# Kernel optimization log

Hardware: AMD Instinct MI355X
Metric: run time of the kernel (lower is better)

The kernel has to match this reference:

```python
import jax, jax.numpy as jnp
import numpy as np
from jax import lax

B, C, H, W = 32, 3, 32, 32
F = 160      # nr_filters
NBLK = 5     # nr_resnet
NMIX = 10    # mixture components
P = 100      # nr_params for 3-channel input


def concat_elu(x):
    return jax.nn.elu(jnp.concatenate([x, -x], axis=1))


def _conv(x, w, b, pad):
    y = lax.conv_general_dilated(x, w, (1, 1), pad, dimension_numbers=('NCHW', 'OIHW', 'NCHW'))
    return y + b[None, :, None, None]


def ds_conv(x, w, b):
    # down-shifted conv: causal in vertical direction
    kh, kw = w.shape[2], w.shape[3]
    return _conv(x, w, b, ((kh - 1, 0), ((kw - 1) // 2, (kw - 1) // 2)))


def dr_conv(x, w, b):
    # down-right-shifted conv: causal in vertical and horizontal direction
    kh, kw = w.shape[2], w.shape[3]
    return _conv(x, w, b, ((kh - 1, 0), (kw - 1, 0)))


def down_shift(x):
    return jnp.pad(x, ((0, 0), (0, 0), (1, 0), (0, 0)))[:, :, :-1, :]


def right_shift(x):
    return jnp.pad(x, ((0, 0), (0, 0), (0, 0), (1, 0)))[:, :, :, :-1]


def nin(x, w, b):
    return jnp.einsum('bchw,oc->bohw', x, w) + b[None, :, None, None]


def gated_resnet(x, a, c1w, c1b, ninw, ninb, c2w, c2b, conv_fn):
    c1 = conv_fn(concat_elu(x), c1w, c1b)
    if a is not None:
        c1 = c1 + nin(concat_elu(a), ninw, ninb)
    c2 = conv_fn(concat_elu(c1), c2w, c2b)  # 2F channels
    g1, g2 = jnp.split(c2, 2, axis=1)
    return x + g1 * jax.nn.sigmoid(g2)


def dmll(x, l):
    # discretized mixture logistic loss; x: [B,C,H,W] in [-1,1], l: [B,P,H,W]
    x = jnp.transpose(x, (0, 2, 3, 1))   # BHWC
    l = jnp.transpose(l, (0, 2, 3, 1))   # BHWP
    logit_probs = l[..., :NMIX]
    rest = l[..., NMIX:].reshape(l.shape[:3] + (C, 3 * NMIX))
    means = rest[..., :NMIX]
    log_scales = jnp.maximum(rest[..., NMIX:2 * NMIX], -7.0)
    coeffs = jnp.tanh(rest[..., 2 * NMIX:])
    xe = x[..., None]                    # BHWC1
    m1 = means[..., 0, :]
    m2 = means[..., 1, :] + coeffs[..., 0, :] * xe[..., 0, :]
    m3 = means[..., 2, :] + coeffs[..., 1, :] * xe[..., 0, :] + coeffs[..., 2, :] * xe[..., 1, :]
    means = jnp.stack([m1, m2, m3], axis=3)  # BHWCM
    centered = xe - means
    inv_stdv = jnp.exp(-log_scales)
    plus_in = inv_stdv * (centered + 1.0 / 255.0)
    min_in = inv_stdv * (centered - 1.0 / 255.0)
    cdf_delta = jax.nn.sigmoid(plus_in) - jax.nn.sigmoid(min_in)
    log_cdf_plus = plus_in - jax.nn.softplus(plus_in)
    log_one_minus_cdf_min = -jax.nn.softplus(min_in)
    mid_in = inv_stdv * centered
    log_pdf_mid = mid_in - log_scales - 2.0 * jax.nn.softplus(mid_in)
    log_probs = jnp.where(xe < -0.999, log_cdf_plus,
                jnp.where(xe > 0.999, log_one_minus_cdf_min,
                jnp.where(cdf_delta > 1e-5, jnp.log(jnp.maximum(cdf_delta, 1e-12)),
                          log_pdf_mid - np.float32(np.log(127.5)))))
    log_probs = log_probs.sum(axis=3) + jax.nn.log_softmax(logit_probs, axis=-1)
    return -jnp.sum(jax.nn.logsumexp(log_probs, axis=-1))


def _forward(samples, w_u_init, b_u_init, w_ul_d, b_ul_d, w_ul_dr, b_ul_dr,
             u_c1_w, u_c1_b, u_c2_w, u_c2_b,
             ul_c1_w, ul_c1_b, ul_nin_w, ul_nin_b, ul_c2_w, ul_c2_b,
             nin_out_w, nin_out_b):
    x = samples * 2.0 - 1.0
    # PixelCNN++ pads a constant ones channel onto the input
    xp = jnp.concatenate([x, jnp.ones_like(x[:, :1])], axis=1)
    u = down_shift(ds_conv(xp, w_u_init, b_u_init))
    ul = down_shift(ds_conv(xp, w_ul_d, b_ul_d)) + right_shift(dr_conv(xp, w_ul_dr, b_ul_dr))
    for i in range(NBLK):
        u = gated_resnet(u, None, u_c1_w[i], u_c1_b[i], None, None, u_c2_w[i], u_c2_b[i], ds_conv)
        ul = gated_resnet(ul, u, ul_c1_w[i], ul_c1_b[i], ul_nin_w[i], ul_nin_b[i], ul_c2_w[i], ul_c2_b[i], dr_conv)
    params = nin(jax.nn.elu(ul), nin_out_w, nin_out_b)  # [B,P,H,W]
    return -dmll(x, params)  # log_prob (scalar, summed over batch/pixels)


def setup_inputs() -> dict:
    key = jax.random.key(0)
    ks = jax.random.split(key, 12)
    s = 0.05
    return {
        'samples': jax.random.uniform(ks[0], (B, C, H, W), jnp.float32),
        'w_u_init': jax.random.normal(ks[1], (F, C + 1, 2, 3), jnp.float32) * s,
        'b_u_init': jnp.zeros((F,), jnp.float32),
        'w_ul_d': jax.random.normal(ks[2], (F, C + 1, 1, 3), jnp.float32) * s,
        'b_ul_d': jnp.zeros((F,), jnp.float32),
        'w_ul_dr': jax.random.normal(ks[3], (F, C + 1, 2, 1), jnp.float32) * s,
        'b_ul_dr': jnp.zeros((F,), jnp.float32),
        'u_c1_w': jax.random.normal(ks[4], (NBLK, F, 2 * F, 2, 3), jnp.float32) * s,
        'u_c1_b': jnp.zeros((NBLK, F), jnp.float32),
        'u_c2_w': jax.random.normal(ks[5], (NBLK, 2 * F, 2 * F, 2, 3), jnp.float32) * s,
        'u_c2_b': jnp.zeros((NBLK, 2 * F), jnp.float32),
        'ul_c1_w': jax.random.normal(ks[6], (NBLK, F, 2 * F, 2, 2), jnp.float32) * s,
        'ul_c1_b': jnp.zeros((NBLK, F), jnp.float32),
        'ul_nin_w': jax.random.normal(ks[7], (NBLK, F, 2 * F), jnp.float32) * s,
        'ul_nin_b': jnp.zeros((NBLK, F), jnp.float32),
        'ul_c2_w': jax.random.normal(ks[8], (NBLK, 2 * F, 2 * F, 2, 2), jnp.float32) * s,
        'ul_c2_b': jnp.zeros((NBLK, 2 * F), jnp.float32),
        'nin_out_w': jax.random.normal(ks[9], (P, F), jnp.float32) * s,
        'nin_out_b': jnp.zeros((P,), jnp.float32),
    }


def reference(samples, w_u_init, b_u_init, w_ul_d, b_ul_d, w_ul_dr, b_ul_dr,
              u_c1_w, u_c1_b, u_c2_w, u_c2_b,
              ul_c1_w, ul_c1_b, ul_nin_w, ul_nin_b, ul_c2_w, ul_c2_b,
              nin_out_w, nin_out_b):
    return _forward(samples, w_u_init, b_u_init, w_ul_d, b_ul_d, w_ul_dr, b_ul_dr,
                    u_c1_w, u_c1_b, u_c2_w, u_c2_b,
                    ul_c1_w, ul_c1_b, ul_nin_w, ul_nin_b, ul_c2_w, ul_c2_b,
                    nin_out_w, nin_out_b)
```

## Files before the change

kernel.cpp:

```cpp
#include <hip/hip_runtime.h>
#include <math.h>

#define BZ 32
#define FCH 160
#define NMIX 10
#define PCH 100

typedef __attribute__((ext_vector_type(8))) short bf16x8;
typedef __attribute__((ext_vector_type(8))) unsigned short u16x8;
typedef __attribute__((ext_vector_type(4))) unsigned short u16x4;
typedef __attribute__((ext_vector_type(4))) float f32x4;

__device__ __forceinline__ unsigned short f2bf(float f) {
    union { float f; unsigned u; } x; x.f = f;
    return (unsigned short)((x.u + 0x7FFFu + ((x.u >> 16) & 1u)) >> 16);
}
__device__ __forceinline__ void elupair(float v, float& e0, float& e1) {
    if (v > 0.f) { e0 = v; e1 = expm1f(-v); }
    else         { e0 = expm1f(v); e1 = -v; }
}
__device__ __forceinline__ int fsw(int p) { return (p + (p >> 2)) & 3; }
__device__ __forceinline__ int swz(int p, int seg) {
    return p * 32 + ((seg ^ fsw(p)) << 3);
}
__device__ __forceinline__ void load_lds16(const unsigned short* g, unsigned short* l) {
    __builtin_amdgcn_global_load_lds(
        (const __attribute__((address_space(1))) unsigned int*)g,
        (__attribute__((address_space(3))) unsigned int*)l, 16, 0, 0);
}

__global__ __launch_bounds__(256) void repack_k(
    const float* __restrict__ w, unsigned short* __restrict__ wb,
    int Cout, int Cin, int NT, int ILV)
{
    __shared__ float ws[1920];
    const int o = blockIdx.x;
    const int nb = blockIdx.y;
    const int CoutPad = gridDim.x;
    const int n = Cin * NT;
    unsigned short* dst = wb + (size_t)(nb * CoutPad + o) * n;
    if (o >= Cout) {
        for (int e = threadIdx.x; e < n; e += 256) dst[e] = 0;
        return;
    }
    const float* src = w + (size_t)(nb * Cout + o) * n;
    for (int e = threadIdx.x; e < n; e += 256) ws[e] = src[e];
    __syncthreads();
    const int half = Cin >> 1;
    for (int e = threadIdx.x; e < n; e += 256) {
        int tap = e / Cin;
        int k = e - tap * Cin;
        int csrc = ILV ? ((k & 1) ? (half + (k >> 1)) : (k >> 1)) : k;
        dst[e] = f2bf(ws[csrc * NT + tap]);
    }
}

__global__ __launch_bounds__(256) void init_both_k(
    const float* __restrict__ smp,
    const float* __restrict__ wu_g, const float* __restrict__ bu_g,
    const float* __restrict__ wd_g, const float* __restrict__ bd_g,
    const float* __restrict__ wr_g, const float* __restrict__ br_g,
    float* __restrict__ u, float* __restrict__ ul,
    unsigned short* __restrict__ ceu, unsigned short* __restrict__ ceul,
    float* __restrict__ zg)
{
    __shared__ float wU[160 * 24];
    __shared__ float wD[160 * 12];
    __shared__ float wR[160 * 8];
    __shared__ float bU[160], bD[160], bR[160];
    __shared__ float X[3][4][34];

    const int tid = threadIdx.x;
    const int i = blockIdx.x;
    const int b = blockIdx.y;

    if (i == 0 && b == 0 && tid < 128) {
        f32x4 z = {0.f, 0.f, 0.f, 0.f};
        ((f32x4*)zg)[tid] = z;
    }

    for (int e = tid; e < 160 * 24; e += 256) wU[e] = wu_g[e];
    for (int e = tid; e < 160 * 12; e += 256) wD[e] = wd_g[e];
    for (int e = tid; e < 160 * 8;  e += 256) wR[e] = wr_g[e];
    if (tid < 160) { bU[tid] = bu_g[tid]; bD[tid] = bd_g[tid]; bR[tid] = br_g[tid]; }
    for (int e = tid; e < 3 * 4 * 34; e += 256) {
        int col = e % 34;
        int c = (e / 34) & 3;
        int rs = e / (34 * 4);
        int r = i - 2 + rs;
        int jj = col - 1;
        float v = 0.f;
        if ((unsigned)r < 32u && (unsigned)jj < 32u)
            v = (c < 3) ? (smp[(((size_t)b * 3 + c) << 10) + (r << 5) + jj] * 2.f - 1.f)
                        : 1.f;
        X[rs][c][col] = v;
    }
    __syncthreads();
    if (tid >= 160) return;
    const int o = tid;

    float wu_r[24], wd_r[12], wr_r[8];
#pragma unroll
    for (int q = 0; q < 24; ++q) wu_r[q] = wU[o * 24 + q];
#pragma unroll
    for (int q = 0; q < 12; ++q) wd_r[q] = wD[o * 12 + q];
#pragma unroll
    for (int q = 0; q < 8; ++q)  wr_r[q] = wR[o * 8 + q];
    const float bu_v = (i > 0) ? bU[o] : 0.f;
    const float bd_v = (i >= 1) ? bD[o] : 0.f;
    const float br_v = bR[o];

    for (int j = 0; j < 32; ++j) {
        float su = 0.f, sd = 0.f, sr = 0.f;
#pragma unroll
        for (int c = 0; c < 4; ++c) {
            float x00 = X[0][c][j], x01 = X[0][c][j + 1], x02 = X[0][c][j + 2];
            float x10 = X[1][c][j], x11 = X[1][c][j + 1], x12 = X[1][c][j + 2];
            float x20 = X[2][c][j];
            su += wu_r[c * 6 + 0] * x00 + wu_r[c * 6 + 1] * x01 + wu_r[c * 6 + 2] * x02
                + wu_r[c * 6 + 3] * x10 + wu_r[c * 6 + 4] * x11 + wu_r[c * 6 + 5] * x12;
            sd += wd_r[c * 3 + 0] * x10 + wd_r[c * 3 + 1] * x11 + wd_r[c * 3 + 2] * x12;
            sr += wr_r[c * 2 + 0] * x10 + wr_r[c * 2 + 1] * x20;
        }
        float uv = (i > 0) ? (su + bu_v) : 0.f;
        float ulv = sd + bd_v + sr + ((j >= 1) ? br_v : 0.f);

        size_t base = (size_t)((b << 10) | (i << 5) | j);
        u[base * 160 + o] = uv;
        ul[base * 160 + o] = ulv;
        float e0, e1;
        elupair(uv, e0, e1);
        unsigned pu = (unsigned)f2bf(e0) | ((unsigned)f2bf(e1) << 16);
        *(unsigned*)(ceu + base * 320 + 2 * o) = pu;
        elupair(ulv, e0, e1);
        unsigned pl = (unsigned)f2bf(e0) | ((unsigned)f2bf(e1) << 16);
        *(unsigned*)(ceul + base * 320 + 2 * o) = pl;
    }
}

template<int KH, int KW, int PT, int PL, bool DUAL, bool GATE, int MBLK>
__device__ __forceinline__ void conv_body(
    int bid, unsigned short* smem,
    const unsigned short* __restrict__ cein,
    const unsigned short* __restrict__ wb,
    const unsigned short* __restrict__ cein2,
    const unsigned short* __restrict__ wb2,
    const float* __restrict__ bias, const float* __restrict__ bias2,
    float* __restrict__ resid,
    unsigned short* __restrict__ ceout,
    const unsigned short* __restrict__ zguard)
{
    constexpr int NT = KH * KW;
    constexpr int RW = 8 + KH - 1;
    constexpr int CW = 32 + KW - 1;
    constexpr int MTILES = MBLK / 16;
    constexpr int MSH = (MBLK == 32) ? 5 : 6;
    constexpr int NSA = NT * MBLK / 64;
    constexpr int NSB = (RW * CW * 4 + 255) / 256;
    constexpr int BSZ = NSB * 64 * 32;

    unsigned short* bs = smem;
    unsigned short* wsm = smem + BSZ;

    const int tid = threadIdx.x;
    const int wv = tid >> 6;
    const int lane = tid & 63;
    const int l16 = lane & 15;
    const int quad = lane >> 4;

    const int q8 = bid >> 3;
    const int yt = (bid & 7) * 16 + q8 / 5;
    const int m0 = (q8 % 5) * 32;
    const int bimg = yt >> 2;
    const int rowbase = (yt & 3) * 8;

    const int sd = lane & 3;
    const int lr = lane >> 2;

    const unsigned short* srcA[NSA];
#pragma unroll
    for (int it = 0; it < NSA; ++it) {
        int row = it * 64 + wv * 16 + lr;
        int tap = row >> MSH;
        int mm = row & (MBLK - 1);
        int o = GATE ? (mm < 32 ? m0 + mm : 128 + m0 + mm) : (m0 + mm);
        int ss = sd ^ fsw(row);
        srcA[it] = wb + ((size_t)o * NT + tap) * 320 + ss * 8;
    }
    const unsigned short* srcB[NSB];
#pragma unroll
    for (int it = 0; it < NSB; ++it) {
        int p = it * 64 + wv * 16 + lr;
        int r = p / CW;
        int c = p - r * CW;
        int grow = rowbase + r - PT;
        int gcol = c - PL;
        int ss = sd ^ fsw(p);
        bool ok = (p < RW * CW) && ((unsigned)grow < 32u) && ((unsigned)gcol < 32u);
        srcB[it] = ok ? cein + (size_t)(((bimg << 10) | (grow << 5) | gcol)) * 320 + ss * 8
                      : zguard;
    }

    f32x4 acc[MTILES][4];
#pragma unroll
    for (int mt = 0; mt < MTILES; ++mt)
#pragma unroll
        for (int ng = 0; ng < 4; ++ng)
#pragma unroll
            for (int r = 0; r < 4; ++r) acc[mt][ng][r] = 0.f;

    for (int k0 = 0; k0 < 320; k0 += 32) {
        __syncthreads();
#pragma unroll
        for (int it = 0; it < NSB; ++it)
            load_lds16(srcB[it] + k0, &bs[(it * 64 + wv * 16) * 32]);
#pragma unroll
        for (int it = 0; it < NSA; ++it)
            load_lds16(srcA[it] + k0, &wsm[(it * 64 + wv * 16) * 32]);
        __syncthreads();
#pragma unroll
        for (int tap = 0; tap < NT; ++tap) {
            const int kh = tap / KW, kw = tap % KW;
            bf16x8 af[MTILES];
#pragma unroll
            for (int mt = 0; mt < MTILES; ++mt)
                af[mt] = *(const bf16x8*)&wsm[swz(tap * MBLK + mt * 16 + l16, quad)];
#pragma unroll
            for (int ng = 0; ng < 4; ++ng) {
                int rl = 2 * wv + (ng >> 1) + kh;
                int cc = (ng & 1) * 16 + l16 + kw;
                bf16x8 bfr = *(const bf16x8*)&bs[swz(rl * CW + cc, quad)];
#pragma unroll
                for (int mt = 0; mt < MTILES; ++mt)
                    acc[mt][ng] = __builtin_amdgcn_mfma_f32_16x16x32_bf16(af[mt], bfr, acc[mt][ng], 0, 0, 0);
            }
        }
    }

    if (DUAL) {
        const unsigned short* srcB2[4];
#pragma unroll
        for (int it = 0; it < 4; ++it) {
            int p2 = it * 64 + wv * 16 + lr;
            int r = p2 >> 5, c = p2 & 31;
            int ss = sd ^ fsw(p2);
            srcB2[it] = cein2 + (size_t)(((bimg << 10) | ((rowbase + r) << 5) | c)) * 320 + ss * 8;
        }
        int row2 = wv * 16 + lr;
        int mm2 = row2 & 31;
        const unsigned short* srcA2 =
            wb2 + (size_t)(m0 + mm2) * 320 + (sd ^ fsw(row2)) * 8;

        for (int k0 = 0; k0 < 320; k0 += 32) {
            __syncthreads();
#pragma unroll
            for (int it = 0; it < 4; ++it)
                load_lds16(srcB2[it] + k0, &bs[(it * 64 + wv * 16) * 32]);
            if (wv < 2)
                load_lds16(srcA2 + k0, &wsm[(wv * 16) * 32]);
            __syncthreads();
            bf16x8 af[MTILES];
#pragma unroll
            for (int mt = 0; mt < MTILES; ++mt)
                af[mt] = *(const bf16x8*)&wsm[swz(mt * 16 + l16, quad)];
#pragma unroll
            for (int ng = 0; ng < 4; ++ng) {
                int rl = 2 * wv + (ng >> 1);
                int cc = (ng & 1) * 16 + l16;
                bf16x8 bfr = *(const bf16x8*)&bs[swz(rl * 32 + cc, quad)];
#pragma unroll
                for (int mt = 0; mt < MTILES; ++mt)
                    acc[mt][ng] = __builtin_amdgcn_mfma_f32_16x16x32_bf16(af[mt], bfr, acc[mt][ng], 0, 0, 0);
            }
        }
    }

    constexpr int MOUT = GATE ? MTILES / 2 : MTILES;
#pragma unroll
    for (int mt = 0; mt < MOUT; ++mt) {
        int ob = m0 + mt * 16 + quad * 4;
        f32x4 bv = *(const f32x4*)(bias + ob);
        f32x4 bv2;
        if (DUAL) bv2 = *(const f32x4*)(bias2 + ob);
        f32x4 bg;
        if (GATE) bg = *(const f32x4*)(bias + ob + 160);
#pragma unroll
        for (int ng = 0; ng < 4; ++ng) {
            int i = rowbase + 2 * wv + (ng >> 1);
            int j = (ng & 1) * 16 + l16;
            size_t pb = (size_t)((bimg << 10) | (i << 5) | j);
            if (!GATE) {
                u16x8 st;
#pragma unroll
                for (int r = 0; r < 4; ++r) {
                    float v = acc[mt][ng][r] + bv[r] + (DUAL ? bv2[r] : 0.f);
                    float e0, e1; elupair(v, e0, e1);
                    st[2 * r] = f2bf(e0); st[2 * r + 1] = f2bf(e1);
                }
                *(u16x8*)(ceout + pb * 320 + 2 * ob) = st;
            } else {
                f32x4 rv = *(const f32x4*)(resid + pb * 160 + ob);
                u16x8 st;
#pragma unroll
                for (int r = 0; r < 4; ++r) {
                    float g1 = acc[mt][ng][r] + bv[r];
                    float g2 = acc[mt + MTILES / 2][ng][r] + bg[r];
                    float v = rv[r] + g1 / (1.f + expf(-g2));
                    rv[r] = v;
                    float e0, e1; elupair(v, e0, e1);
                    st[2 * r] = f2bf(e0); st[2 * r + 1] = f2bf(e1);
                }
                *(f32x4*)(resid + pb * 160 + ob) = rv;
                *(u16x8*)(ceout + pb * 320 + 2 * ob) = st;
            }
        }
    }
}

template<int KH, int KW, int PT, int PL, bool DUAL, bool GATE, int MBLK>
__global__ __launch_bounds__(256) void conv_single_k(
    const unsigned short* __restrict__ cein, const unsigned short* __restrict__ wb,
    const unsigned short* __restrict__ cein2, const unsigned short* __restrict__ wb2,
    const float* __restrict__ bias, const float* __restrict__ bias2,
    float* __restrict__ resid, unsigned short* __restrict__ ceout,
    const unsigned short* __restrict__ zguard)
{
    extern __shared__ __align__(16) unsigned short dsm[];
    conv_body<KH, KW, PT, PL, DUAL, GATE, MBLK>(
        blockIdx.x, dsm, cein, wb, cein2, wb2, bias, bias2, resid, ceout, zguard);
}

__global__ __launch_bounds__(256) void conv_fused_c1_k(
    const unsigned short* __restrict__ ceul, const unsigned short* __restrict__ wul1,
    const unsigned short* __restrict__ ceu_nin, const unsigned short* __restrict__ wnin,
    const float* __restrict__ bul1, const float* __restrict__ bnin,
    unsigned short* __restrict__ cec1ul,
    const unsigned short* __restrict__ ceu, const unsigned short* __restrict__ wu1,
    const float* __restrict__ bu1, unsigned short* __restrict__ cec1u,
    const unsigned short* __restrict__ zguard)
{
    extern __shared__ __align__(16) unsigned short dsm[];
    if (blockIdx.x < 640)
        conv_body<2, 2, 1, 1, true, false, 32>(
            blockIdx.x, dsm, ceul, wul1, ceu_nin, wnin, bul1, bnin, nullptr, cec1ul, zguard);
    else
        conv_body<2, 3, 1, 1, false, false, 32>(
            blockIdx.x - 640, dsm, ceu, wu1, nullptr, nullptr, bu1, nullptr, nullptr, cec1u, zguard);
}

__global__ __launch_bounds__(256) void conv_fused_c2_k(
    const unsigned short* __restrict__ cec1ul, const unsigned short* __restrict__ wul2,
    const float* __restrict__ bul2, float* __restrict__ ul_r,
    unsigned short* __restrict__ ceul,
    const unsigned short* __restrict__ cec1u, const unsigned short* __restrict__ wu2,
    const float* __restrict__ bu2, float* __restrict__ u_r,
    unsigned short* __restrict__ ceu,
    const unsigned short* __restrict__ zguard)
{
    extern __shared__ __align__(16) unsigned short dsm[];
    if (blockIdx.x < 640)
        conv_body<2, 2, 1, 1, false, true, 64>(
            blockIdx.x, dsm, cec1ul, wul2, nullptr, nullptr, bul2, nullptr, ul_r, ceul, zguard);
    else
        conv_body<2, 3, 1, 1, false, true, 64>(
            blockIdx.x - 640, dsm, cec1u, wu2, nullptr, nullptr, bu2, nullptr, u_r, ceu, zguard);
}

__global__ __launch_bounds__(256) void ninout_k(
    const float* __restrict__ ul, const unsigned short* __restrict__ wbn,
    const float* __restrict__ bias, float* __restrict__ params)
{
    constexpr int KCP = 40;
    __shared__ __align__(16) unsigned short bs[256 * KCP];
    __shared__ __align__(16) unsigned short wsm[32 * KCP];

    const int tid = threadIdx.x;
    const int wv = tid >> 6;
    const int lane = tid & 63;
    const int l16 = lane & 15;
    const int quad = lane >> 4;
    const int m0 = blockIdx.x * 32;
    const int bimg = blockIdx.y >> 2;
    const int rowbase = (blockIdx.y & 3) * 8;

    f32x4 acc[2][4];
#pragma unroll
    for (int mt = 0; mt < 2; ++mt)
#pragma unroll
        for (int ng = 0; ng < 4; ++ng)
#pragma unroll
            for (int r = 0; r < 4; ++r) acc[mt][ng][r] = 0.f;

    for (int k0 = 0; k0 < 160; k0 += 32) {
        __syncthreads();
        for (int e = tid; e < 256 * 8; e += 256) {
            int s = e & 7;
            int p = e >> 3;
            int pix = ((rowbase + (p >> 5)) << 5) | (p & 31);
            f32x4 xv = *(const f32x4*)(ul + (size_t)(((bimg << 10) | pix)) * 160 + k0 + s * 4);
            u16x4 st;
#pragma unroll
            for (int t = 0; t < 4; ++t) {
                float v = xv[t];
                st[t] = f2bf(v > 0.f ? v : expm1f(v));
            }
            *(u16x4*)(bs + p * KCP + s * 4) = st;
        }
        for (int e = tid; e < 32 * 4; e += 256) {
            int seg = e & 3;
            int mm = e >> 2;
            bf16x8 v = *(const bf16x8*)(wbn + (size_t)(m0 + mm) * 160 + k0 + seg * 8);
            *(bf16x8*)(wsm + mm * KCP + seg * 8) = v;
        }
        __syncthreads();
        bf16x8 af[2];
#pragma unroll
        for (int mt = 0; mt < 2; ++mt)
            af[mt] = *(const bf16x8*)&wsm[(mt * 16 + l16) * KCP + quad * 8];
#pragma unroll
        for (int ng = 0; ng < 4; ++ng) {
            int rl = 2 * wv + (ng >> 1);
            int cc = (ng & 1) * 16 + l16;
            bf16x8 bfr = *(const bf16x8*)&bs[(rl * 32 + cc) * KCP + quad * 8];
#pragma unroll
            for (int mt = 0; mt < 2; ++mt)
                acc[mt][ng] = __builtin_amdgcn_mfma_f32_16x16x32_bf16(af[mt], bfr, acc[mt][ng], 0, 0, 0);
        }
    }
#pragma unroll
    for (int mt = 0; mt < 2; ++mt)
#pragma unroll
        for (int ng = 0; ng < 4; ++ng) {
            int i = rowbase + 2 * wv + (ng >> 1);
            int j = (ng & 1) * 16 + l16;
            int pix = (i << 5) + j;
#pragma unroll
            for (int r = 0; r < 4; ++r) {
                int o = m0 + mt * 16 + quad * 4 + r;
                if (o < PCH)
                    params[(((size_t)bimg * PCH + o) << 10) + pix] = acc[mt][ng][r] + bias[o];
            }
        }
}

__device__ __forceinline__ float softplus_f(float v) {
    return fmaxf(v, 0.f) + log1pf(expf(-fabsf(v)));
}
__device__ __forceinline__ float sigmoid_f(float v) { return 1.f / (1.f + expf(-v)); }
__device__ __forceinline__ float lpterm(float x, float m, float ls) {
    float inv = expf(-ls);
    float cen = x - m;
    float plus = inv * (cen + 0.00392156862745098f);
    float minv = inv * (cen - 0.00392156862745098f);
    float cdf_delta = sigmoid_f(plus) - sigmoid_f(minv);
    float log_cdf_plus = plus - softplus_f(plus);
    float log_om = -softplus_f(minv);
    float mid = inv * cen;
    float log_pdf_mid = mid - ls - 2.f * softplus_f(mid);
    float inner = (cdf_delta > 1e-5f) ? logf(fmaxf(cdf_delta, 1e-12f))
                                      : (log_pdf_mid - 4.848116389675623f);
    return (x < -0.999f) ? log_cdf_plus : ((x > 0.999f) ? log_om : inner);
}

__global__ __launch_bounds__(256) void dmll_k(
    const float* __restrict__ smp, const float* __restrict__ params,
    float* __restrict__ partials)
{
    const int tid = threadIdx.x;
    const int n = tid & 15;
    const int ploc = tid >> 4;
    const int pix_g = blockIdx.x * 16 + ploc;
    const int b = pix_g >> 10;
    const int ij = pix_g & 1023;
    const float* P = params + ((size_t)b * PCH << 10) + ij;

    float x0 = smp[(((size_t)b * 3 + 0) << 10) + ij] * 2.f - 1.f;
    float x1 = smp[(((size_t)b * 3 + 1) << 10) + ij] * 2.f - 1.f;
    float x2 = smp[(((size_t)b * 3 + 2) << 10) + ij] * 2.f - 1.f;

    float logit = -1e30f;
    if (n < NMIX) logit = P[(size_t)n << 10];
    float mx = logit;
#pragma unroll
    for (int m = 1; m < 16; m <<= 1) mx = fmaxf(mx, __shfl_xor(mx, m, 16));
    float ex = (n < NMIX) ? expf(logit - mx) : 0.f;
    float se = ex;
#pragma unroll
    for (int m = 1; m < 16; m <<= 1) se += __shfl_xor(se, m, 16);
    float lse_logit = mx + logf(se);

    float lp = -1e30f;
    if (n < NMIX) {
        float mean0 = P[(size_t)(10 + n) << 10];
        float mean1 = P[(size_t)(40 + n) << 10];
        float mean2 = P[(size_t)(70 + n) << 10];
        float ls0 = fmaxf(P[(size_t)(20 + n) << 10], -7.f);
        float ls1 = fmaxf(P[(size_t)(50 + n) << 10], -7.f);
        float ls2 = fmaxf(P[(size_t)(80 + n) << 10], -7.f);
        float c0 = tanhf(P[(size_t)(30 + n) << 10]);
        float c1 = tanhf(P[(size_t)(60 + n) << 10]);
        float c2 = tanhf(P[(size_t)(90 + n) << 10]);
        float m0 = mean0;
        float m1 = mean1 + c0 * x0;
        float m2 = mean2 + c1 * x0 + c2 * x1;
        float s3 = lpterm(x0, m0, ls0) + lpterm(x1, m1, ls1) + lpterm(x2, m2, ls2);
        lp = s3 + logit - lse_logit;
    }
    float mx2 = lp;
#pragma unroll
    for (int m = 1; m < 16; m <<= 1) mx2 = fmaxf(mx2, __shfl_xor(mx2, m, 16));
    float e2 = (n < NMIX) ? expf(lp - mx2) : 0.f;
    float se2 = e2;
#pragma unroll
    for (int m = 1; m < 16; m <<= 1) se2 += __shfl_xor(se2, m, 16);
    float v = (n == 0) ? (mx2 + logf(se2)) : 0.f;

#pragma unroll
    for (int off = 32; off > 0; off >>= 1) v += __shfl_down(v, off);
    __shared__ float red[4];
    if ((tid & 63) == 0) red[tid >> 6] = v;
    __syncthreads();
    if (tid == 0) partials[blockIdx.x] = red[0] + red[1] + red[2] + red[3];
}

__global__ __launch_bounds__(256) void dmll_final_k(
    const float* __restrict__ partials, float* __restrict__ out)
{
    float v = 0.f;
    for (int k = threadIdx.x; k < 2048; k += 256) v += partials[k];
#pragma unroll
    for (int off = 32; off > 0; off >>= 1) v += __shfl_down(v, off);
    __shared__ float red[4];
    if ((threadIdx.x & 63) == 0) red[threadIdx.x >> 6] = v;
    __syncthreads();
    if (threadIdx.x == 0) out[0] = red[0] + red[1] + red[2] + red[3];
}

extern "C" void kernel_launch(void* const* d_in, const int* in_sizes, int n_in,
                              void* d_out, int out_size, void* d_ws, size_t ws_size,
                              hipStream_t stream)
{
    const float* samples   = (const float*)d_in[0];
    const float* w_u_init  = (const float*)d_in[1];
    const float* b_u_init  = (const float*)d_in[2];
    const float* w_ul_d    = (const float*)d_in[3];
    const float* b_ul_d    = (const float*)d_in[4];
    const float* w_ul_dr   = (const float*)d_in[5];
    const float* b_ul_dr   = (const float*)d_in[6];
    const float* u_c1_w    = (const float*)d_in[7];
    const float* u_c1_b    = (const float*)d_in[8];
    const float* u_c2_w    = (const float*)d_in[9];
    const float* u_c2_b    = (const float*)d_in[10];
    const float* ul_c1_w   = (const float*)d_in[11];
    const float* ul_c1_b   = (const float*)d_in[12];
    const float* ul_nin_w  = (const float*)d_in[13];
    const float* ul_nin_b  = (const float*)d_in[14];
    const float* ul_c2_w   = (const float*)d_in[15];
    const float* ul_c2_b   = (const float*)d_in[16];
    const float* nin_out_w = (const float*)d_in[17];
    const float* nin_out_b = (const float*)d_in[18];
    float* out = (float*)d_out;

    const size_t NU = (size_t)BZ * FCH * 1024;
    float* u  = (float*)d_ws;
    float* ul = u + NU;
    unsigned short* CEu    = (unsigned short*)(ul + NU);
    unsigned short* CEc1u  = CEu + 2 * NU;
    unsigned short* CEc1ul = CEc1u + 2 * NU;
    unsigned short* CEul   = CEc1ul + 2 * NU;
    unsigned short* WBu1  = CEul + 2 * NU;
    unsigned short* WBu2  = WBu1 + (size_t)5 * 160 * 6 * 320;
    unsigned short* WBul1 = WBu2 + (size_t)5 * 320 * 6 * 320;
    unsigned short* WBnin = WBul1 + (size_t)5 * 160 * 4 * 320;
    unsigned short* WBul2 = WBnin + (size_t)5 * 160 * 1 * 320;
    unsigned short* WBnout = WBul2 + (size_t)5 * 320 * 4 * 320;
    float* partials = (float*)(WBnout + (size_t)128 * 160);
    float* zguard = partials + 2048;
    float* params = (float*)CEc1u;

    dim3 blk(256);

    const int SH_UC1  = (5 * 64 * 32 + 6 * 32 * 32) * 2;
    const int SH_UC2  = (5 * 64 * 32 + 6 * 64 * 32) * 2;
    const int SH_ULC1 = (5 * 64 * 32 + 4 * 32 * 32) * 2;
    const int SH_ULC2 = (5 * 64 * 32 + 4 * 64 * 32) * 2;
    const int SH_F1 = SH_UC1;
    const int SH_F2 = SH_UC2;

    repack_k<<<dim3(160, 5), blk, 0, stream>>>(u_c1_w,    WBu1,  160, 320, 6, 1);
    repack_k<<<dim3(320, 5), blk, 0, stream>>>(u_c2_w,    WBu2,  320, 320, 6, 1);
    repack_k<<<dim3(160, 5), blk, 0, stream>>>(ul_c1_w,   WBul1, 160, 320, 4, 1);
    repack_k<<<dim3(160, 5), blk, 0, stream>>>(ul_nin_w,  WBnin, 160, 320, 1, 1);
    repack_k<<<dim3(320, 5), blk, 0, stream>>>(ul_c2_w,   WBul2, 320, 320, 4, 1);
    repack_k<<<dim3(128, 1), blk, 0, stream>>>(nin_out_w, WBnout, 100, 160, 1, 0);

    init_both_k<<<dim3(32, 32), blk, 0, stream>>>(
        samples, w_u_init, b_u_init, w_ul_d, b_ul_d, w_ul_dr, b_ul_dr,
        u, ul, CEu, CEul, zguard);

    const unsigned short* zg = (const unsigned short*)zguard;

    conv_single_k<2, 3, 1, 1, false, false, 32><<<640, blk, SH_UC1, stream>>>(
        CEu, WBu1, nullptr, nullptr, u_c1_b, nullptr, nullptr, CEc1u, zg);
    conv_single_k<2, 3, 1, 1, false, true, 64><<<640, blk, SH_UC2, stream>>>(
        CEc1u, WBu2, nullptr, nullptr, u_c2_b, nullptr, u, CEu, zg);

    for (int t = 0; t < 4; ++t) {
        conv_fused_c1_k<<<1280, blk, SH_F1, stream>>>(
            CEul, WBul1 + (size_t)t * 160 * 4 * 320,
            CEu, WBnin + (size_t)t * 160 * 320,
            ul_c1_b + t * 160, ul_nin_b + t * 160, CEc1ul,
            CEu, WBu1 + (size_t)(t + 1) * 160 * 6 * 320,
            u_c1_b + (t + 1) * 160, CEc1u, zg);
        conv_fused_c2_k<<<1280, blk, SH_F2, stream>>>(
            CEc1ul, WBul2 + (size_t)t * 320 * 4 * 320,
            ul_c2_b + t * 320, ul, CEul,
            CEc1u, WBu2 + (size_t)(t + 1) * 320 * 6 * 320,
            u_c2_b + (t + 1) * 320, u, CEu, zg);
    }

    conv_single_k<2, 2, 1, 1, true, false, 32><<<640, blk, SH_ULC1, stream>>>(
        CEul, WBul1 + (size_t)4 * 160 * 4 * 320, CEu, WBnin + (size_t)4 * 160 * 320,
        ul_c1_b + 4 * 160, ul_nin_b + 4 * 160, nullptr, CEc1ul, zg);
    conv_single_k<2, 2, 1, 1, false, true, 64><<<640, blk, SH_ULC2, stream>>>(
        CEc1ul, WBul2 + (size_t)4 * 320 * 4 * 320, nullptr, nullptr,
        ul_c2_b + 4 * 320, nullptr, ul, CEul, zg);

    ninout_k<<<dim3(4, 128), blk, 0, stream>>>(ul, WBnout, nin_out_b, params);
    dmll_k<<<2048, blk, 0, stream>>>(samples, params, partials);
    dmll_final_k<<<1, 256, 0, stream>>>(partials, out);
}
```

Measured before the change: 987.2 us.

## Split conv tile across 8 waves by M to halve per-wave accumulators

Conv kernels now launch 512 threads (8 waves) instead of 256, splitting the output-channel tiles between two wave groups so each wave holds half the accumulators and issues half the MFMAs per tile. Global-to-LDS staging is redistributed over 8 waves with bounds guards, and LDS sizing is recomputed. The aim is more waves per block for latency hiding and lower register pressure. In exchange, B fragments are read from LDS twice (once per wave group) and block-wide syncs cover more waves.

```diff
diff --git a/kernel.cpp b/kernel.cpp
--- a/kernel.cpp
+++ b/kernel.cpp
@@ -154,16 +154,19 @@
     constexpr int RW = 8 + KH - 1;
     constexpr int CW = 32 + KW - 1;
     constexpr int MTILES = MBLK / 16;
+    constexpr int MTW = MTILES / 2;
     constexpr int MSH = (MBLK == 32) ? 5 : 6;
-    constexpr int NSA = NT * MBLK / 64;
-    constexpr int NSB = (RW * CW * 4 + 255) / 256;
-    constexpr int BSZ = NSB * 64 * 32;
+    constexpr int NSA = (NT * MBLK + 127) / 128;
+    constexpr int NSB = (RW * CW + 127) / 128;
+    constexpr int BROWS = 320;
 
     unsigned short* bs = smem;
-    unsigned short* wsm = smem + BSZ;
+    unsigned short* wsm = smem + BROWS * 32;
 
     const int tid = threadIdx.x;
-    const int wv = tid >> 6;
+    const int wv8 = tid >> 6;
+    const int wq = wv8 & 3;
+    const int wm = wv8 >> 2;
     const int lane = tid & 63;
     const int l16 = lane & 15;
     const int quad = lane >> 4;
@@ -178,19 +181,25 @@
     const int lr = lane >> 2;
 
     const unsigned short* srcA[NSA];
+    bool okA[NSA];
 #pragma unroll
     for (int it = 0; it < NSA; ++it) {
-        int row = it * 64 + wv * 16 + lr;
-        int tap = row >> MSH;
+        int base = it * 128 + (wv8 << 4);
+        okA[it] = base < NT * MBLK;
+        int row = base + lr;
+        int tap = (row >> MSH) % NT;
         int mm = row & (MBLK - 1);
         int o = GATE ? (mm < 32 ? m0 + mm : 128 + m0 + mm) : (m0 + mm);
         int ss = sd ^ fsw(row);
         srcA[it] = wb + ((size_t)o * NT + tap) * 320 + ss * 8;
     }
     const unsigned short* srcB[NSB];
+    bool okB[NSB];
 #pragma unroll
     for (int it = 0; it < NSB; ++it) {
-        int p = it * 64 + wv * 16 + lr;
+        int base = it * 128 + (wv8 << 4);
+        okB[it] = base < RW * CW;
+        int p = base + lr;
         int r = p / CW;
         int c = p - r * CW;
         int grow = rowbase + r - PT;
@@ -201,52 +210,54 @@
                       : zguard;
     }
 
-    f32x4 acc[MTILES][4];
-#pragma unroll
-    for (int mt = 0; mt < MTILES; ++mt)
+    f32x4 acc[MTW][4];
+#pragma unroll
+    for (int k = 0; k < MTW; ++k)
 #pragma unroll
         for (int ng = 0; ng < 4; ++ng)
 #pragma unroll
-            for (int r = 0; r < 4; ++r) acc[mt][ng][r] = 0.f;
+            for (int r = 0; r < 4; ++r) acc[k][ng][r] = 0.f;
 
     for (int k0 = 0; k0 < 320; k0 += 32) {
         __syncthreads();
 #pragma unroll
         for (int it = 0; it < NSB; ++it)
-            load_lds16(srcB[it] + k0, &bs[(it * 64 + wv * 16) * 32]);
+            if (okB[it])
+                load_lds16(srcB[it] + k0, &bs[(it * 128 + (wv8 << 4)) * 32]);
 #pragma unroll
         for (int it = 0; it < NSA; ++it)
-            load_lds16(srcA[it] + k0, &wsm[(it * 64 + wv * 16) * 32]);
+            if (okA[it])
+                load_lds16(srcA[it] + k0, &wsm[(it * 128 + (wv8 << 4)) * 32]);
         __syncthreads();
 #pragma unroll
         for (int tap = 0; tap < NT; ++tap) {
             const int kh = tap / KW, kw = tap % KW;
-            bf16x8 af[MTILES];
-#pragma unroll
-            for (int mt = 0; mt < MTILES; ++mt)
-                af[mt] = *(const bf16x8*)&wsm[swz(tap * MBLK + mt * 16 + l16, quad)];
+            bf16x8 af[MTW];
+#pragma unroll
+            for (int k = 0; k < MTW; ++k)
+                af[k] = *(const bf16x8*)&wsm[swz(tap * MBLK + (wm + 2 * k) * 16 + l16, quad)];
 #pragma unroll
             for (int ng = 0; ng < 4; ++ng) {
-                int rl = 2 * wv + (ng >> 1) + kh;
+                int rl = 2 * wq + (ng >> 1) + kh;
                 int cc = (ng & 1) * 16 + l16 + kw;
                 bf16x8 bfr = *(const bf16x8*)&bs[swz(rl * CW + cc, quad)];
 #pragma unroll
-                for (int mt = 0; mt < MTILES; ++mt)
-                    acc[mt][ng] = __builtin_amdgcn_mfma_f32_16x16x32_bf16(af[mt], bfr, acc[mt][ng], 0, 0, 0);
+                for (int k = 0; k < MTW; ++k)
+                    acc[k][ng] = __builtin_amdgcn_mfma_f32_16x16x32_bf16(af[k], bfr, acc[k][ng], 0, 0, 0);
             }
         }
     }
 
     if (DUAL) {
-        const unsigned short* srcB2[4];
-#pragma unroll
-        for (int it = 0; it < 4; ++it) {
-            int p2 = it * 64 + wv * 16 + lr;
+        const unsigned short* srcB2[2];
+#pragma unroll
+        for (int it = 0; it < 2; ++it) {
+            int p2 = it * 128 + (wv8 << 4) + lr;
             int r = p2 >> 5, c = p2 & 31;
             int ss = sd ^ fsw(p2);
             srcB2[it] = cein2 + (size_t)(((bimg << 10) | ((rowbase + r) << 5) | c)) * 320 + ss * 8;
         }
-        int row2 = wv * 16 + lr;
+        int row2 = (wv8 << 4) + lr;
         int mm2 = row2 & 31;
         const unsigned short* srcA2 =
             wb2 + (size_t)(m0 + mm2) * 320 + (sd ^ fsw(row2)) * 8;
@@ -254,31 +265,24 @@
         for (int k0 = 0; k0 < 320; k0 += 32) {
             __syncthreads();
 #pragma unroll
-            for (int it = 0; it < 4; ++it)
-                load_lds16(srcB2[it] + k0, &bs[(it * 64 + wv * 16) * 32]);
-            if (wv < 2)
-                load_lds16(srcA2 + k0, &wsm[(wv * 16) * 32]);
+            for (int it = 0; it < 2; ++it)
+                load_lds16(srcB2[it] + k0, &bs[(it * 128 + (wv8 << 4)) * 32]);
+            if (wv8 < 2)
+                load_lds16(srcA2 + k0, &wsm[(wv8 << 4) * 32]);
             __syncthreads();
-            bf16x8 af[MTILES];
-#pragma unroll
-            for (int mt = 0; mt < MTILES; ++mt)
-                af[mt] = *(const bf16x8*)&wsm[swz(mt * 16 + l16, quad)];
+            bf16x8 af2 = *(const bf16x8*)&wsm[swz(wm * 16 + l16, quad)];
 #pragma unroll
             for (int ng = 0; ng < 4; ++ng) {
-                int rl = 2 * wv + (ng >> 1);
+                int rl = 2 * wq + (ng >> 1);
                 int cc = (ng & 1) * 16 + l16;
                 bf16x8 bfr = *(const bf16x8*)&bs[swz(rl * 32 + cc, quad)];
-#pragma unroll
-                for (int mt = 0; mt < MTILES; ++mt)
-                    acc[mt][ng] = __builtin_amdgcn_mfma_f32_16x16x32_bf16(af[mt], bfr, acc[mt][ng], 0, 0, 0);
+                acc[0][ng] = __builtin_amdgcn_mfma_f32_16x16x32_bf16(af2, bfr, acc[0][ng], 0, 0, 0);
             }
         }
     }
 
-    constexpr int MOUT = GATE ? MTILES / 2 : MTILES;
-#pragma unroll
-    for (int mt = 0; mt < MOUT; ++mt) {
-        int ob = m0 + mt * 16 + quad * 4;
+    {
+        int ob = m0 + wm * 16 + quad * 4;
         f32x4 bv = *(const f32x4*)(bias + ob);
         f32x4 bv2;
         if (DUAL) bv2 = *(const f32x4*)(bias2 + ob);
@@ -286,14 +290,14 @@
         if (GATE) bg = *(const f32x4*)(bias + ob + 160);
 #pragma unroll
         for (int ng = 0; ng < 4; ++ng) {
-            int i = rowbase + 2 * wv + (ng >> 1);
+            int i = rowbase + 2 * wq + (ng >> 1);
             int j = (ng & 1) * 16 + l16;
             size_t pb = (size_t)((bimg << 10) | (i << 5) | j);
             if (!GATE) {
                 u16x8 st;
 #pragma unroll
                 for (int r = 0; r < 4; ++r) {
-                    float v = acc[mt][ng][r] + bv[r] + (DUAL ? bv2[r] : 0.f);
+                    float v = acc[0][ng][r] + bv[r] + (DUAL ? bv2[r] : 0.f);
                     float e0, e1; elupair(v, e0, e1);
                     st[2 * r] = f2bf(e0); st[2 * r + 1] = f2bf(e1);
                 }
@@ -303,8 +307,8 @@
                 u16x8 st;
 #pragma unroll
                 for (int r = 0; r < 4; ++r) {
-                    float g1 = acc[mt][ng][r] + bv[r];
-                    float g2 = acc[mt + MTILES / 2][ng][r] + bg[r];
+                    float g1 = acc[0][ng][r] + bv[r];
+                    float g2 = acc[1][ng][r] + bg[r];
                     float v = rv[r] + g1 / (1.f + expf(-g2));
                     rv[r] = v;
                     float e0, e1; elupair(v, e0, e1);
@@ -318,7 +322,7 @@
 }
 
 template<int KH, int KW, int PT, int PL, bool DUAL, bool GATE, int MBLK>
-__global__ __launch_bounds__(256) void conv_single_k(
+__global__ __launch_bounds__(512) void conv_single_k(
     const unsigned short* __restrict__ cein, const unsigned short* __restrict__ wb,
     const unsigned short* __restrict__ cein2, const unsigned short* __restrict__ wb2,
     const float* __restrict__ bias, const float* __restrict__ bias2,
@@ -330,7 +334,7 @@
         blockIdx.x, dsm, cein, wb, cein2, wb2, bias, bias2, resid, ceout, zguard);
 }
 
-__global__ __launch_bounds__(256) void conv_fused_c1_k(
+__global__ __launch_bounds__(512) void conv_fused_c1_k(
     const unsigned short* __restrict__ ceul, const unsigned short* __restrict__ wul1,
     const unsigned short* __restrict__ ceu_nin, const unsigned short* __restrict__ wnin,
     const float* __restrict__ bul1, const float* __restrict__ bnin,
@@ -348,7 +352,7 @@
             blockIdx.x - 640, dsm, ceu, wu1, nullptr, nullptr, bu1, nullptr, nullptr, cec1u, zguard);
 }
 
-__global__ __launch_bounds__(256) void conv_fused_c2_k(
+__global__ __launch_bounds__(512) void conv_fused_c2_k(
     const unsigned short* __restrict__ cec1ul, const unsigned short* __restrict__ wul2,
     const float* __restrict__ bul2, float* __restrict__ ul_r,
     unsigned short* __restrict__ ceul,
@@ -579,11 +583,12 @@
     float* params = (float*)CEc1u;
 
     dim3 blk(256);
-
-    const int SH_UC1  = (5 * 64 * 32 + 6 * 32 * 32) * 2;
-    const int SH_UC2  = (5 * 64 * 32 + 6 * 64 * 32) * 2;
-    const int SH_ULC1 = (5 * 64 * 32 + 4 * 32 * 32) * 2;
-    const int SH_ULC2 = (5 * 64 * 32 + 4 * 64 * 32) * 2;
+    dim3 cblk(512);
+
+    const int SH_UC1  = (320 + 192) * 64;
+    const int SH_UC2  = (320 + 384) * 64;
+    const int SH_ULC1 = (320 + 128) * 64;
+    const int SH_ULC2 = (320 + 256) * 64;
     const int SH_F1 = SH_UC1;
     const int SH_F2 = SH_UC2;
 
@@ -600,29 +605,29 @@
 
     const unsigned short* zg = (const unsigned short*)zguard;
 
-    conv_single_k<2, 3, 1, 1, false, false, 32><<<640, blk, SH_UC1, stream>>>(
+    conv_single_k<2, 3, 1, 1, false, false, 32><<<640, cblk, SH_UC1, stream>>>(
         CEu, WBu1, nullptr, nullptr, u_c1_b, nullptr, nullptr, CEc1u, zg);
-    conv_single_k<2, 3, 1, 1, false, true, 64><<<640, blk, SH_UC2, stream>>>(
+    conv_single_k<2, 3, 1, 1, false, true, 64><<<640, cblk, SH_UC2, stream>>>(
         CEc1u, WBu2, nullptr, nullptr, u_c2_b, nullptr, u, CEu, zg);
 
     for (int t = 0; t < 4; ++t) {
-        conv_fused_c1_k<<<1280, blk, SH_F1, stream>>>(
+        conv_fused_c1_k<<<1280, cblk, SH_F1, stream>>>(
             CEul, WBul1 + (size_t)t * 160 * 4 * 320,
             CEu, WBnin + (size_t)t * 160 * 320,
             ul_c1_b + t * 160, ul_nin_b + t * 160, CEc1ul,
             CEu, WBu1 + (size_t)(t + 1) * 160 * 6 * 320,
             u_c1_b + (t + 1) * 160, CEc1u, zg);
-        conv_fused_c2_k<<<1280, blk, SH_F2, stream>>>(
+        conv_fused_c2_k<<<1280, cblk, SH_F2, stream>>>(
             CEc1ul, WBul2 + (size_t)t * 320 * 4 * 320,
             ul_c2_b + t * 320, ul, CEul,
             CEc1u, WBu2 + (size_t)(t + 1) * 320 * 6 * 320,
             u_c2_b + (t + 1) * 320, u, CEu, zg);
     }
 
-    conv_single_k<2, 2, 1, 1, true, false, 32><<<640, blk, SH_ULC1, stream>>>(
+    conv_single_k<2, 2, 1, 1, true, false, 32><<<640, cblk, SH_ULC1, stream>>>(
         CEul, WBul1 + (size_t)4 * 160 * 4 * 320, CEu, WBnin + (size_t)4 * 160 * 320,
         ul_c1_b + 4 * 160, ul_nin_b + 4 * 160, nullptr, CEc1ul, zg);
-    conv_single_k<2, 2, 1, 1, false, true, 64><<<640, blk, SH_ULC2, stream>>>(
+    conv_single_k<2, 2, 1, 1, false, true, 64><<<640, cblk, SH_ULC2, stream>>>(
         CEc1ul, WBul2 + (size_t)4 * 320 * 4 * 320, nullptr, nullptr,
         ul_c2_b + 4 * 320, nullptr, ul, CEul, zg);
 
```

Result: no change. 1.002 ms (+1.5%).
